# Optimization experiments

Measured on AMD Instinct MI355X. Metric: run time of the kernel, lower is better.

The kernel has to match this reference:

```python
import jax, jax.numpy as jnp
import numpy as np

EPS = 1e-12

def setup_inputs() -> dict:
    key = jax.random.key(0)
    k1, k2, k3, k4 = jax.random.split(key, 4)
    B, L, D = 32, 2048, 64
    q = jax.random.normal(k1, (B, L, D), dtype=jnp.float32)
    k = jax.random.normal(k2, (B, L, D), dtype=jnp.float32)
    v = jax.random.normal(k3, (B, L, D), dtype=jnp.float32)
    mask = jax.random.randint(k4, (B, L, L), 0, 2) > 0  # True = masked out
    return {"q": q, "k": k, "v": v, "mask": mask}

def reference(q, k, v, mask):
    # L2-normalize q and k along feature dim (clamped like torch .clamp(min=1e-12))
    q_n = q / jnp.clip(jnp.linalg.norm(q, axis=2, keepdims=True), EPS, None)
    k_n = k / jnp.clip(jnp.linalg.norm(k, axis=2, keepdims=True), EPS, None)
    # cosine similarity scores shifted into [0, 2]
    attn = jnp.einsum('bqd,bkd->bqk', q_n, k_n) + 1.0
    attn = jnp.where(mask, 0.0, attn)
    # sum-normalize instead of softmax
    attn = attn / jnp.clip(jnp.sum(attn, axis=2, keepdims=True), EPS, None)
    # dropout is identity in eval / p=0
    output = jnp.einsum('bqk,bkd->bqd', attn, v)
    return (output, attn)
```

## Files before the change

kernel.cpp:

```cpp
#include <hip/hip_runtime.h>
#include <hip/hip_bf16.h>
#include <stdint.h>

#define Bn 32
#define Ln 2048
#define Dn 64

typedef __bf16 bf16x8_t __attribute__((ext_vector_type(8)));
typedef float f32x4_t __attribute__((ext_vector_type(4)));

__device__ __forceinline__ int swzi(int row, int col) {
  return (((row << 7) + (col << 1)) ^ ((row & 7) << 4)) >> 1;
}

__device__ __forceinline__ void stage_norm_tile(const float* __restrict__ src,
                                                __bf16* dst, int tid) {
#pragma unroll
  for (int half = 0; half < 2; ++half) {
    const int chunk = half * 256 + tid;
    const int row = chunk >> 3, h = chunk & 7;
    const float4* p = (const float4*)(src + row * 64 + h * 8);
    float4 x0 = p[0], x1 = p[1];
    float ss = x0.x * x0.x + x0.y * x0.y + x0.z * x0.z + x0.w * x0.w +
               x1.x * x1.x + x1.y * x1.y + x1.z * x1.z + x1.w * x1.w;
    ss += __shfl_xor(ss, 1);
    ss += __shfl_xor(ss, 2);
    ss += __shfl_xor(ss, 4);
    const float inv = 1.0f / fmaxf(sqrtf(ss), 1e-12f);
    bf16x8_t hv;
    hv[0] = (__bf16)(x0.x * inv); hv[1] = (__bf16)(x0.y * inv);
    hv[2] = (__bf16)(x0.z * inv); hv[3] = (__bf16)(x0.w * inv);
    hv[4] = (__bf16)(x1.x * inv); hv[5] = (__bf16)(x1.y * inv);
    hv[6] = (__bf16)(x1.z * inv); hv[7] = (__bf16)(x1.w * inv);
    *(bf16x8_t*)&dst[swzi(row, h * 8)] = hv;
  }
}

__device__ __forceinline__ void stage_v_T(const float* __restrict__ src,
                                          __bf16* dst, int tid) {
  const int krow = tid >> 2, seg = tid & 3;
  const float4* p = (const float4*)(src + krow * 64) + seg * 4;
#pragma unroll
  for (int j = 0; j < 4; ++j) {
    float4 x = p[j];
    const int f = seg * 16 + j * 4;
    dst[swzi(f + 0, krow)] = (__bf16)x.x;
    dst[swzi(f + 1, krow)] = (__bf16)x.y;
    dst[swzi(f + 2, krow)] = (__bf16)x.z;
    dst[swzi(f + 3, krow)] = (__bf16)x.w;
  }
}

__global__ __launch_bounds__(256, 4)
void cosattn_kernel(const float* __restrict__ q, const float* __restrict__ kk,
                    const float* __restrict__ v, const int* __restrict__ mask,
                    float* __restrict__ out, float* __restrict__ attn) {
  __shared__ __align__(16) __bf16 QS[4096];
  __shared__ __align__(16) __bf16 KN[4096];
  __shared__ __align__(16) __bf16 VT[4096];
  __shared__ uint16_t BITS[64 * 128];

  const int tid = threadIdx.x;
  const int wid = tid >> 6;
  const int lane = tid & 63;
  const int c = lane & 15;
  const int g = lane >> 4;

  const int bid = blockIdx.x;
  const int flat = (bid & 7) * 128 + (bid >> 3);
  const int b = flat >> 5;
  const int qt = flat & 31;

  const float* qb = q + ((size_t)b * Ln + (size_t)qt * 64) * Dn;
  const float* kb = kk + (size_t)b * Ln * Dn;
  const float* vb = v + (size_t)b * Ln * Dn;
  const int* mb = mask + (size_t)b * Ln * Ln + (size_t)qt * 64 * Ln;
  float* attnb = attn + (size_t)b * Ln * Ln;

  stage_norm_tile(qb, QS, tid);

#pragma unroll 4
  for (int it = 0; it < 32; ++it) {
    const int wi = it * 256 + tid;
    const uint4* p = (const uint4*)(mb + wi * 16);
    unsigned w = 0;
#pragma unroll
    for (int j = 0; j < 4; ++j) {
      uint4 x = p[j];
      w |= ((x.x & 1u) | ((x.y & 1u) << 1) | ((x.z & 1u) << 2) | ((x.w & 1u) << 3)) << (j * 4);
    }
    BITS[wi] = (uint16_t)w;
  }
  __syncthreads();

  bf16x8_t a0 = *(const bf16x8_t*)&QS[swzi(wid * 16 + c, g * 8)];
  bf16x8_t a1 = *(const bf16x8_t*)&QS[swzi(wid * 16 + c, 32 + g * 8)];

  float rsum[4] = {0.f, 0.f, 0.f, 0.f};
  for (int kt = 0; kt < 32; ++kt) {
    __syncthreads();
    stage_norm_tile(kb + kt * 4096, KN, tid);
    __syncthreads();
#pragma unroll
    for (int ct = 0; ct < 4; ++ct) {
      bf16x8_t b0 = *(const bf16x8_t*)&KN[swzi(ct * 16 + c, g * 8)];
      bf16x8_t b1 = *(const bf16x8_t*)&KN[swzi(ct * 16 + c, 32 + g * 8)];
      f32x4_t acc = {0.f, 0.f, 0.f, 0.f};
      acc = __builtin_amdgcn_mfma_f32_16x16x32_bf16(a0, b0, acc, 0, 0, 0);
      acc = __builtin_amdgcn_mfma_f32_16x16x32_bf16(a1, b1, acc, 0, 0, 0);
#pragma unroll
      for (int r = 0; r < 4; ++r) {
        const int qrl = wid * 16 + g * 4 + r;
        const unsigned w = BITS[qrl * 128 + kt * 4 + ct];
        const float s = ((w >> c) & 1u) ? 0.f : (acc[r] + 1.f);
        rsum[r] += s;
      }
    }
  }
  float invr[4];
#pragma unroll
  for (int r = 0; r < 4; ++r) {
    float s = rsum[r];
    s += __shfl_xor(s, 1); s += __shfl_xor(s, 2);
    s += __shfl_xor(s, 4); s += __shfl_xor(s, 8);
    invr[r] = 1.0f / fmaxf(s, 1e-12f);
  }

  f32x4_t oacc[4] = {{0.f,0.f,0.f,0.f},{0.f,0.f,0.f,0.f},{0.f,0.f,0.f,0.f},{0.f,0.f,0.f,0.f}};
  __bf16* SL = QS + wid * 1024;
  for (int kt = 0; kt < 32; ++kt) {
    __syncthreads();
    stage_norm_tile(kb + kt * 4096, KN, tid);
    stage_v_T(vb + kt * 4096, VT, tid);
    __syncthreads();
#pragma unroll
    for (int ct = 0; ct < 4; ++ct) {
      bf16x8_t b0 = *(const bf16x8_t*)&KN[swzi(ct * 16 + c, g * 8)];
      bf16x8_t b1 = *(const bf16x8_t*)&KN[swzi(ct * 16 + c, 32 + g * 8)];
      f32x4_t acc = {0.f, 0.f, 0.f, 0.f};
      acc = __builtin_amdgcn_mfma_f32_16x16x32_bf16(a0, b0, acc, 0, 0, 0);
      acc = __builtin_amdgcn_mfma_f32_16x16x32_bf16(a1, b1, acc, 0, 0, 0);
#pragma unroll
      for (int r = 0; r < 4; ++r) {
        const int qrl = wid * 16 + g * 4 + r;
        const unsigned w = BITS[qrl * 128 + kt * 4 + ct];
        const float s = ((w >> c) & 1u) ? 0.f : (acc[r] + 1.f);
        const float av = s * invr[r];
        attnb[(size_t)(qt * 64 + qrl) * Ln + kt * 64 + ct * 16 + c] = av;
        SL[swzi(g * 4 + r, ct * 16 + c)] = (__bf16)av;
      }
    }
    bf16x8_t sa0 = *(const bf16x8_t*)&SL[swzi(c, g * 8)];
    bf16x8_t sa1 = *(const bf16x8_t*)&SL[swzi(c, 32 + g * 8)];
#pragma unroll
    for (int nt = 0; nt < 4; ++nt) {
      bf16x8_t vb0 = *(const bf16x8_t*)&VT[swzi(nt * 16 + c, g * 8)];
      bf16x8_t vb1 = *(const bf16x8_t*)&VT[swzi(nt * 16 + c, 32 + g * 8)];
      oacc[nt] = __builtin_amdgcn_mfma_f32_16x16x32_bf16(sa0, vb0, oacc[nt], 0, 0, 0);
      oacc[nt] = __builtin_amdgcn_mfma_f32_16x16x32_bf16(sa1, vb1, oacc[nt], 0, 0, 0);
    }
  }

  float* ob = out + ((size_t)b * Ln + (size_t)qt * 64) * Dn;
#pragma unroll
  for (int nt = 0; nt < 4; ++nt)
#pragma unroll
    for (int r = 0; r < 4; ++r)
      ob[(wid * 16 + g * 4 + r) * 64 + nt * 16 + c] = oacc[nt][r];
}

extern "C" void kernel_launch(void* const* d_in, const int* in_sizes, int n_in,
                              void* d_out, int out_size, void* d_ws, size_t ws_size,
                              hipStream_t stream) {
  const float* q = (const float*)d_in[0];
  const float* k = (const float*)d_in[1];
  const float* v = (const float*)d_in[2];
  const int* mask = (const int*)d_in[3];
  float* out = (float*)d_out;
  float* attn = out + (size_t)Bn * Ln * Dn;
  dim3 grid(Bn * (Ln / 64));
  cosattn_kernel<<<grid, 256, 0, stream>>>(q, k, v, mask, out, attn);
}
```

Before: 1.101 ms.

## Prefetch K/V tiles into registers and double-buffer K in shared memory

Splits tile staging into a global load into registers and a later normalize-and-store, so the next K (and V) tile's global loads are issued before the current tile's MFMA work. K is double-buffered in LDS, and the Q tile is held temporarily in the VT buffer, which keeps LDS usage similar. The mask bitmap is repacked into 32-bit words with an XOR-swizzled layout, and each row's bits are loaded once per k-tile. This is meant to hide global load latency, at the cost of more registers, which could reduce occupancy under launch_bounds(256,4).

```diff
diff --git a/kernel.cpp b/kernel.cpp
--- a/kernel.cpp
+++ b/kernel.cpp
@@ -13,36 +13,61 @@
   return (((row << 7) + (col << 1)) ^ ((row & 7) << 4)) >> 1;
 }
 
-__device__ __forceinline__ void stage_norm_tile(const float* __restrict__ src,
-                                                __bf16* dst, int tid) {
-#pragma unroll
-  for (int half = 0; half < 2; ++half) {
-    const int chunk = half * 256 + tid;
+__device__ __forceinline__ int bidx(int w32, int row) {
+  return (w32 << 6) | (row ^ (w32 & 31));
+}
+
+struct TileRegs { float4 a0, b0, a1, b1; };
+
+__device__ __forceinline__ void load_tile(const float* __restrict__ src, int tid, TileRegs& t) {
+  {
+    const int row = tid >> 3, h = tid & 7;
+    const float4* p = (const float4*)(src + row * 64 + h * 8);
+    t.a0 = p[0]; t.b0 = p[1];
+  }
+  {
+    const int chunk = 256 + tid;
     const int row = chunk >> 3, h = chunk & 7;
     const float4* p = (const float4*)(src + row * 64 + h * 8);
-    float4 x0 = p[0], x1 = p[1];
-    float ss = x0.x * x0.x + x0.y * x0.y + x0.z * x0.z + x0.w * x0.w +
-               x1.x * x1.x + x1.y * x1.y + x1.z * x1.z + x1.w * x1.w;
-    ss += __shfl_xor(ss, 1);
-    ss += __shfl_xor(ss, 2);
-    ss += __shfl_xor(ss, 4);
-    const float inv = 1.0f / fmaxf(sqrtf(ss), 1e-12f);
-    bf16x8_t hv;
-    hv[0] = (__bf16)(x0.x * inv); hv[1] = (__bf16)(x0.y * inv);
-    hv[2] = (__bf16)(x0.z * inv); hv[3] = (__bf16)(x0.w * inv);
-    hv[4] = (__bf16)(x1.x * inv); hv[5] = (__bf16)(x1.y * inv);
-    hv[6] = (__bf16)(x1.z * inv); hv[7] = (__bf16)(x1.w * inv);
-    *(bf16x8_t*)&dst[swzi(row, h * 8)] = hv;
-  }
-}
-
-__device__ __forceinline__ void stage_v_T(const float* __restrict__ src,
-                                          __bf16* dst, int tid) {
+    t.a1 = p[0]; t.b1 = p[1];
+  }
+}
+
+__device__ __forceinline__ void finish_half(float4 x0, float4 x1, __bf16* dst, int row, int h) {
+  float ss = x0.x * x0.x + x0.y * x0.y + x0.z * x0.z + x0.w * x0.w +
+             x1.x * x1.x + x1.y * x1.y + x1.z * x1.z + x1.w * x1.w;
+  ss += __shfl_xor(ss, 1);
+  ss += __shfl_xor(ss, 2);
+  ss += __shfl_xor(ss, 4);
+  const float inv = 1.0f / fmaxf(sqrtf(ss), 1e-12f);
+  bf16x8_t hv;
+  hv[0] = (__bf16)(x0.x * inv); hv[1] = (__bf16)(x0.y * inv);
+  hv[2] = (__bf16)(x0.z * inv); hv[3] = (__bf16)(x0.w * inv);
+  hv[4] = (__bf16)(x1.x * inv); hv[5] = (__bf16)(x1.y * inv);
+  hv[6] = (__bf16)(x1.z * inv); hv[7] = (__bf16)(x1.w * inv);
+  *(bf16x8_t*)&dst[swzi(row, h * 8)] = hv;
+}
+
+__device__ __forceinline__ void finish_tile(const TileRegs& t, __bf16* dst, int tid) {
+  finish_half(t.a0, t.b0, dst, tid >> 3, tid & 7);
+  const int chunk = 256 + tid;
+  finish_half(t.a1, t.b1, dst, chunk >> 3, chunk & 7);
+}
+
+struct VRegs { float4 y0, y1, y2, y3; };
+
+__device__ __forceinline__ void load_v(const float* __restrict__ src, int tid, VRegs& v) {
   const int krow = tid >> 2, seg = tid & 3;
   const float4* p = (const float4*)(src + krow * 64) + seg * 4;
+  v.y0 = p[0]; v.y1 = p[1]; v.y2 = p[2]; v.y3 = p[3];
+}
+
+__device__ __forceinline__ void finish_v(const VRegs& v, __bf16* dst, int tid) {
+  const int krow = tid >> 2, seg = tid & 3;
+  const float4 ys[4] = {v.y0, v.y1, v.y2, v.y3};
 #pragma unroll
   for (int j = 0; j < 4; ++j) {
-    float4 x = p[j];
+    const float4 x = ys[j];
     const int f = seg * 16 + j * 4;
     dst[swzi(f + 0, krow)] = (__bf16)x.x;
     dst[swzi(f + 1, krow)] = (__bf16)x.y;
@@ -55,10 +80,9 @@
 void cosattn_kernel(const float* __restrict__ q, const float* __restrict__ kk,
                     const float* __restrict__ v, const int* __restrict__ mask,
                     float* __restrict__ out, float* __restrict__ attn) {
-  __shared__ __align__(16) __bf16 QS[4096];
-  __shared__ __align__(16) __bf16 KN[4096];
+  __shared__ __align__(16) __bf16 KN[2][4096];
   __shared__ __align__(16) __bf16 VT[4096];
-  __shared__ uint16_t BITS[64 * 128];
+  __shared__ unsigned BITS32[4096];
 
   const int tid = threadIdx.x;
   const int wid = tid >> 6;
@@ -77,46 +101,63 @@
   const int* mb = mask + (size_t)b * Ln * Ln + (size_t)qt * 64 * Ln;
   float* attnb = attn + (size_t)b * Ln * Ln;
 
-  stage_norm_tile(qb, QS, tid);
-
-#pragma unroll 4
-  for (int it = 0; it < 32; ++it) {
-    const int wi = it * 256 + tid;
-    const uint4* p = (const uint4*)(mb + wi * 16);
-    unsigned w = 0;
-#pragma unroll
-    for (int j = 0; j < 4; ++j) {
+  TileRegs qr, kr;
+  load_tile(qb, tid, qr);
+  load_tile(kb, tid, kr);
+
+#pragma unroll 2
+  for (int it = 0; it < 16; ++it) {
+    const int f = it * 256 + tid;
+    const int qrow = f >> 6, w32 = f & 63;
+    const uint4* p = (const uint4*)(mb + qrow * 2048 + w32 * 32);
+    unsigned m = 0;
+#pragma unroll
+    for (int j = 0; j < 8; ++j) {
       uint4 x = p[j];
-      w |= ((x.x & 1u) | ((x.y & 1u) << 1) | ((x.z & 1u) << 2) | ((x.w & 1u) << 3)) << (j * 4);
-    }
-    BITS[wi] = (uint16_t)w;
-  }
+      m |= ((x.x & 1u) | ((x.y & 1u) << 1) | ((x.z & 1u) << 2) | ((x.w & 1u) << 3)) << (j * 4);
+    }
+    BITS32[bidx(w32, qrow)] = m;
+  }
+
+  finish_tile(qr, VT, tid);
+  finish_tile(kr, KN[0], tid);
   __syncthreads();
 
-  bf16x8_t a0 = *(const bf16x8_t*)&QS[swzi(wid * 16 + c, g * 8)];
-  bf16x8_t a1 = *(const bf16x8_t*)&QS[swzi(wid * 16 + c, 32 + g * 8)];
+  bf16x8_t a0 = *(const bf16x8_t*)&VT[swzi(wid * 16 + c, g * 8)];
+  bf16x8_t a1 = *(const bf16x8_t*)&VT[swzi(wid * 16 + c, 32 + g * 8)];
 
   float rsum[4] = {0.f, 0.f, 0.f, 0.f};
   for (int kt = 0; kt < 32; ++kt) {
-    __syncthreads();
-    stage_norm_tile(kb + kt * 4096, KN, tid);
-    __syncthreads();
+    const int cur = kt & 1;
+    if (kt < 31) load_tile(kb + (kt + 1) * 4096, tid, kr);
+    const __bf16* KC = KN[cur];
+    unsigned mr[4][2];
+#pragma unroll
+    for (int r = 0; r < 4; ++r) {
+      const int qrl = wid * 16 + g * 4 + r;
+      mr[r][0] = BITS32[bidx(2 * kt, qrl)];
+      mr[r][1] = BITS32[bidx(2 * kt + 1, qrl)];
+    }
 #pragma unroll
     for (int ct = 0; ct < 4; ++ct) {
-      bf16x8_t b0 = *(const bf16x8_t*)&KN[swzi(ct * 16 + c, g * 8)];
-      bf16x8_t b1 = *(const bf16x8_t*)&KN[swzi(ct * 16 + c, 32 + g * 8)];
+      bf16x8_t b0 = *(const bf16x8_t*)&KC[swzi(ct * 16 + c, g * 8)];
+      bf16x8_t b1 = *(const bf16x8_t*)&KC[swzi(ct * 16 + c, 32 + g * 8)];
       f32x4_t acc = {0.f, 0.f, 0.f, 0.f};
       acc = __builtin_amdgcn_mfma_f32_16x16x32_bf16(a0, b0, acc, 0, 0, 0);
       acc = __builtin_amdgcn_mfma_f32_16x16x32_bf16(a1, b1, acc, 0, 0, 0);
 #pragma unroll
       for (int r = 0; r < 4; ++r) {
-        const int qrl = wid * 16 + g * 4 + r;
-        const unsigned w = BITS[qrl * 128 + kt * 4 + ct];
-        const float s = ((w >> c) & 1u) ? 0.f : (acc[r] + 1.f);
-        rsum[r] += s;
+        const unsigned bit = (mr[r][ct >> 1] >> (((ct & 1) << 4) + c)) & 1u;
+        rsum[r] += bit ? 0.f : (acc[r] + 1.f);
       }
     }
-  }
+    __syncthreads();
+    if (kt < 31) {
+      finish_tile(kr, KN[cur ^ 1], tid);
+      __syncthreads();
+    }
+  }
+
   float invr[4];
 #pragma unroll
   for (int r = 0; r < 4; ++r) {
@@ -126,25 +167,41 @@
     invr[r] = 1.0f / fmaxf(s, 1e-12f);
   }
 
+  VRegs vr;
+  load_tile(kb, tid, kr);
+  load_v(vb, tid, vr);
+  finish_tile(kr, KN[0], tid);
+  finish_v(vr, VT, tid);
+  __syncthreads();
+
   f32x4_t oacc[4] = {{0.f,0.f,0.f,0.f},{0.f,0.f,0.f,0.f},{0.f,0.f,0.f,0.f},{0.f,0.f,0.f,0.f}};
-  __bf16* SL = QS + wid * 1024;
   for (int kt = 0; kt < 32; ++kt) {
-    __syncthreads();
-    stage_norm_tile(kb + kt * 4096, KN, tid);
-    stage_v_T(vb + kt * 4096, VT, tid);
-    __syncthreads();
+    const int cur = kt & 1;
+    if (kt < 31) {
+      load_tile(kb + (kt + 1) * 4096, tid, kr);
+      load_v(vb + (kt + 1) * 4096, tid, vr);
+    }
+    const __bf16* KC = KN[cur];
+    __bf16* SL = (__bf16*)KN[cur ^ 1] + wid * 1024;
+    unsigned mr[4][2];
+#pragma unroll
+    for (int r = 0; r < 4; ++r) {
+      const int qrl = wid * 16 + g * 4 + r;
+      mr[r][0] = BITS32[bidx(2 * kt, qrl)];
+      mr[r][1] = BITS32[bidx(2 * kt + 1, qrl)];
+    }
 #pragma unroll
     for (int ct = 0; ct < 4; ++ct) {
-      bf16x8_t b0 = *(const bf16x8_t*)&KN[swzi(ct * 16 + c, g * 8)];
-      bf16x8_t b1 = *(const bf16x8_t*)&KN[swzi(ct * 16 + c, 32 + g * 8)];
+      bf16x8_t b0 = *(const bf16x8_t*)&KC[swzi(ct * 16 + c, g * 8)];
+      bf16x8_t b1 = *(const bf16x8_t*)&KC[swzi(ct * 16 + c, 32 + g * 8)];
       f32x4_t acc = {0.f, 0.f, 0.f, 0.f};
       acc = __builtin_amdgcn_mfma_f32_16x16x32_bf16(a0, b0, acc, 0, 0, 0);
       acc = __builtin_amdgcn_mfma_f32_16x16x32_bf16(a1, b1, acc, 0, 0, 0);
 #pragma unroll
       for (int r = 0; r < 4; ++r) {
         const int qrl = wid * 16 + g * 4 + r;
-        const unsigned w = BITS[qrl * 128 + kt * 4 + ct];
-        const float s = ((w >> c) & 1u) ? 0.f : (acc[r] + 1.f);
+        const unsigned bit = (mr[r][ct >> 1] >> (((ct & 1) << 4) + c)) & 1u;
+        const float s = bit ? 0.f : (acc[r] + 1.f);
         const float av = s * invr[r];
         attnb[(size_t)(qt * 64 + qrl) * Ln + kt * 64 + ct * 16 + c] = av;
         SL[swzi(g * 4 + r, ct * 16 + c)] = (__bf16)av;
@@ -158,6 +215,12 @@
       bf16x8_t vb1 = *(const bf16x8_t*)&VT[swzi(nt * 16 + c, 32 + g * 8)];
       oacc[nt] = __builtin_amdgcn_mfma_f32_16x16x32_bf16(sa0, vb0, oacc[nt], 0, 0, 0);
       oacc[nt] = __builtin_amdgcn_mfma_f32_16x16x32_bf16(sa1, vb1, oacc[nt], 0, 0, 0);
+    }
+    __syncthreads();
+    if (kt < 31) {
+      finish_tile(kr, KN[cur ^ 1], tid);
+      finish_v(vr, VT, tid);
+      __syncthreads();
     }
   }
 
```

Result: slower. 1.154 ms (+4.8%).
